# Kernel tuning notes

Measured on AMD Instinct MI355X. Metric: run time of the kernel, lower is better.

The kernel has to match this reference:

```python
import jax, jax.numpy as jnp
import numpy as np

B, P, E, D, A, M, V, T = 64, 196, 2048, 512, 512, 512, 10000, 31


def setup_inputs() -> dict:
    key = jax.random.key(0)
    ks = jax.random.split(key, 20)
    s = 0.02
    inp = {
        "encoder_out": jax.random.normal(ks[0], (B, P, E), jnp.float32),
        "captions": jax.random.randint(ks[1], (B, T), 0, V),
        "caption_lengths": jax.random.randint(ks[2], (B,), 2, T + 1).at[0].set(T),
        # parameters
        "W_emb": jax.random.normal(ks[3], (V, M), jnp.float32) * s,
        "We": jax.random.normal(ks[4], (A, E), jnp.float32) * s,
        "be": jnp.zeros((A,), jnp.float32),
        "Wd": jax.random.normal(ks[5], (A, D), jnp.float32) * s,
        "bd": jnp.zeros((A,), jnp.float32),
        "wf": jax.random.normal(ks[6], (1, A), jnp.float32) * s,
        "bf": jnp.zeros((1,), jnp.float32),
        "Wih": jax.random.normal(ks[7], (4 * D, M + E), jnp.float32) * s,
        "bih": jnp.zeros((4 * D,), jnp.float32),
        "Whh": jax.random.normal(ks[8], (4 * D, D), jnp.float32) * s,
        "bhh": jnp.zeros((4 * D,), jnp.float32),
        "Wfc": jax.random.normal(ks[9], (V, D), jnp.float32) * s,
        "bfc": jnp.zeros((V,), jnp.float32),
        "Wh0": jax.random.normal(ks[10], (D, E), jnp.float32) * s,
        "bh0": jnp.zeros((D,), jnp.float32),
        "Wc0": jax.random.normal(ks[11], (D, E), jnp.float32) * s,
        "bc0": jnp.zeros((D,), jnp.float32),
    }
    return inp


def _decode(encoder_out, W_emb, We, be, Wd, bd, wf, bf, Wih, bih, Whh, bhh,
            Wfc, bfc, Wh0, bh0, Wc0, bc0, captions, caption_lengths):
    # sort by length descending (matches torch .sort(descending=True))
    idx = jnp.argsort(-caption_lengths)
    lens = caption_lengths[idx]
    enc = encoder_out[idx]              # [B,P,E]
    caps = captions[idx]                # [B,T]
    emb = W_emb[caps]                   # [B,T,M]
    mean_enc = enc.mean(axis=1)         # [B,E]
    h0 = mean_enc @ Wh0.T + bh0         # [B,D]
    c0 = mean_enc @ Wc0.T + bc0
    dec_len = lens - 1                  # [B]
    att1 = enc @ We.T + be              # [B,P,A] precomputed encoder projection
    Tmax = caps.shape[1] - 1

    def step(carry, xs):
        h, c = carry
        e_t, t = xs                     # e_t: [B,M]
        active = (t < dec_len)          # [B]
        att2 = h @ Wd.T + bd            # [B,A]
        scores = jnp.tanh(att1 + att2[:, None, :]) @ wf[0] + bf[0]  # [B,P]
        alpha = jax.nn.softmax(scores, axis=-1)                      # [B,P]
        ctx = jnp.einsum('bp,bpe->be', alpha, enc)                   # [B,E]
        x = jnp.concatenate([e_t, ctx], axis=-1)                     # [B,M+E]
        gates = x @ Wih.T + bih + h @ Whh.T + bhh                    # [B,4D]
        i_g, f_g, g_g, o_g = jnp.split(gates, 4, axis=-1)
        c_t = jax.nn.sigmoid(f_g) * c + jax.nn.sigmoid(i_g) * jnp.tanh(g_g)
        h_t = jax.nn.sigmoid(o_g) * jnp.tanh(c_t)
        pred = h_t @ Wfc.T + bfc        # dropout in eval mode = identity
        m = active[:, None]
        h_new = jnp.where(m, h_t, h)
        c_new = jnp.where(m, c_t, c)
        pred = jnp.where(m, pred, 0.0)
        alpha = jnp.where(m, alpha, 0.0)
        return (h_new, c_new), (pred, alpha)

    emb_ts = jnp.swapaxes(emb[:, :Tmax, :], 0, 1)  # [Tmax,B,M]
    ts = jnp.arange(Tmax)
    _, (preds, alphas) = jax.lax.scan(step, (h0, c0), (emb_ts, ts))
    predictions = jnp.swapaxes(preds, 0, 1)   # [B,Tmax,V]
    alphas = jnp.swapaxes(alphas, 0, 1)       # [B,Tmax,P]
    return predictions, alphas


def reference(encoder_out, captions, caption_lengths, W_emb, We, be, Wd, bd,
              wf, bf, Wih, bih, Whh, bhh, Wfc, bfc, Wh0, bh0, Wc0, bc0):
    return _decode(encoder_out, W_emb, We, be, Wd, bd, wf, bf, Wih, bih,
                   Whh, bhh, Wfc, bfc, Wh0, bh0, Wc0, bc0,
                   captions, caption_lengths)
```

## Files before the change

kernel.cpp:

```cpp
#include <hip/hip_runtime.h>
#include <cstdint>
#include <cstddef>

typedef __attribute__((ext_vector_type(8))) short short8;
typedef __attribute__((ext_vector_type(4))) float f32x4;

#define DEV static __device__ __forceinline__

#define PRED_ELEMS 19200000ULL

#define OFF_ENC   0ULL
#define OFF_ATT1  51380224ULL
#define OFF_B1    64225280ULL
#define OFF_WFC   69468160ULL
#define OFF_WEB   79724544ULL
#define OFF_B0    81821696ULL
#define OFF_HH    81821696ULL
#define OFF_PA2   83787776ULL
#define OFF_B2    86016000ULL
#define OFF_HX    94404608ULL
#define OFF_C     94535680ULL
#define OFF_GEH   94797824ULL
#define OFF_SC    95322112ULL
#define OFF_CTX   95372288ULL
#define OFF_META  95634432ULL
#define OFF_ENCW  96000000ULL

DEV float b2f(unsigned short u){ unsigned v = ((unsigned)u) << 16; float f; __builtin_memcpy(&f, &v, 4); return f; }
DEV unsigned short f2b(float x){ unsigned v; __builtin_memcpy(&v, &x, 4); unsigned r = v + 0x7fffu + ((v >> 16) & 1u); return (unsigned short)(r >> 16); }
DEV float sigm(float x){ return 1.0f / (1.0f + __expf(-x)); }
DEV float tanhf_fast(float x){ float e = __expf(2.0f * x); return 1.0f - 2.0f / (e + 1.0f); }

DEV void gload16(const void* g, void* l){
  __builtin_amdgcn_global_load_lds((const __attribute__((address_space(1))) unsigned int*)g,
                                   (__attribute__((address_space(3))) unsigned int*)l, 16, 0, 0);
}

DEV void mm_core(const unsigned short* A, int ldA, int m0,
                 const unsigned short* Bm, int ldB, int n0,
                 int kIters, unsigned short* As, unsigned short* Bs, f32x4 acc[4])
{
  const int tid = threadIdx.x;
  const int lane = tid & 63, w = tid >> 6;
  const unsigned short* ga = A + (size_t)(m0 + lane) * ldA + w * 8;
  const unsigned short* gb = Bm + (size_t)(n0 + lane) * ldB + w * 8;
  unsigned short* la = As + w * 512;
  unsigned short* lb = Bs + w * 512;
  const int kb = lane >> 4, rr = lane & 15;
  for (int kk = 0; kk < kIters; ++kk) {
    gload16(ga, la); gload16(gb, lb);
    ga += 32; gb += 32;
    asm volatile("s_waitcnt vmcnt(0)" ::: "memory");
    __syncthreads();
    short8 bfr = *(const short8*)(Bs + (size_t)(kb * 64 + w * 16 + rr) * 8);
#pragma unroll
    for (int f = 0; f < 4; ++f) {
      short8 afr = *(const short8*)(As + (size_t)(kb * 64 + f * 16 + rr) * 8);
      acc[f] = __builtin_amdgcn_mfma_f32_16x16x32_bf16(afr, bfr, acc[f], 0, 0, 0);
    }
    __syncthreads();
  }
}

__global__ void k_meta(const int* __restrict__ caps, const int* __restrict__ lens, int* __restrict__ meta){
  int j = threadIdx.x;
  int lj = lens[j];
  int rank = 0;
  for (int k = 0; k < 64; ++k) { int lk = lens[k]; rank += (lk > lj) || (lk == lj && k < j); }
  meta[rank] = j; meta[64 + rank] = lj - 1;
  for (int t = 0; t < 31; ++t) meta[160 + rank * 31 + t] = caps[j * 31 + t];
  __syncthreads();
  if (j < 30) { int c = 0; for (int b = 0; b < 64; ++b) c += (meta[64 + b] > j); meta[128 + j] = c; }
}

__global__ __launch_bounds__(256) void k_encg(const float* __restrict__ enc, const int* __restrict__ meta, unsigned short* __restrict__ encb){
  int row = blockIdx.x; int b = row / 196, p = row % 196;
  const float* src = enc + ((size_t)meta[b] * 196 + p) * 2048;
  unsigned short* dst = encb + (size_t)row * 2048;
  int e0 = threadIdx.x * 8;
  short8 o;
#pragma unroll
  for (int j = 0; j < 8; ++j) o[j] = (short)f2b(src[e0 + j]);
  *(short8*)(dst + e0) = o;
}

__global__ __launch_bounds__(256) void k_wconv(const float* We, const float* Wh0, const float* Wc0,
                        const float* Wd, const float* Whh, const float* Wih, const float* Wfc,
                        unsigned short* Web, unsigned short* B0, unsigned short* B1,
                        unsigned short* Wfcb, unsigned short* B2){
  int bid = blockIdx.x, tid = threadIdx.x;
  if (bid < 512) {
    const float* s = We + (size_t)bid * 2048; unsigned short* d = Web + (size_t)bid * 2048;
    int e0 = tid * 8; short8 o;
#pragma unroll
    for (int j = 0; j < 8; ++j) o[j] = (short)f2b(s[e0 + j]);
    *(short8*)(d + e0) = o;
  } else if (bid < 1536) {
    int r = bid - 512;
    const float* s = (r < 512) ? (Wh0 + (size_t)r * 2048) : (Wc0 + (size_t)(r - 512) * 2048);
    unsigned short* d = B0 + (size_t)r * 2048;
    int e0 = tid * 8; short8 o;
#pragma unroll
    for (int j = 0; j < 8; ++j) o[j] = (short)f2b(s[e0 + j]);
    *(short8*)(d + e0) = o;
  } else if (bid < 3584) {
    int jr = bid - 1536; int g = (jr & 3) * 512 + (jr >> 2);
    const float* s = Wih + (size_t)g * 2560 + 512;
    unsigned short* d = B2 + (size_t)jr * 2048;
    int e0 = tid * 8; short8 o;
#pragma unroll
    for (int j = 0; j < 8; ++j) o[j] = (short)f2b(s[e0 + j]);
    *(short8*)(d + e0) = o;
  } else if (bid < 6144) {
    int n = bid - 3584; unsigned short* d = B1 + (size_t)n * 1024;
    int k0 = tid * 4;
    if (n < 512) {
#pragma unroll
      for (int j = 0; j < 4; ++j) { int k = k0 + j; d[k] = (k < 512) ? f2b(Wd[(size_t)n * 512 + k]) : (unsigned short)0; }
    } else {
      int j2 = n - 512; int g = (j2 & 3) * 512 + (j2 >> 2);
#pragma unroll
      for (int j = 0; j < 4; ++j) { int k = k0 + j;
        d[k] = (k < 512) ? f2b(Whh[(size_t)g * 512 + k]) : f2b(Wih[(size_t)g * 2560 + (k - 512)]); }
    }
  } else {
    int v = bid - 6144; unsigned short* d = Wfcb + (size_t)v * 512;
    int k0 = tid * 2;
#pragma unroll
    for (int j = 0; j < 2; ++j) d[k0 + j] = (v < 10000) ? f2b(Wfc[(size_t)v * 512 + k0 + j]) : (unsigned short)0;
  }
}

__global__ __launch_bounds__(256) void k_mean(const unsigned short* __restrict__ encb, unsigned short* __restrict__ meanb){
  int b = blockIdx.y, ch = blockIdx.x;
  int e = ch * 512 + threadIdx.x * 2;
  const unsigned short* ep = encb + (size_t)b * 196 * 2048 + e;
  float s0 = 0.f, s1 = 0.f;
  for (int p = 0; p < 196; ++p) {
    unsigned u = *(const unsigned*)(ep + (size_t)p * 2048);
    s0 += b2f((unsigned short)(u & 0xffff));
    s1 += b2f((unsigned short)(u >> 16));
  }
  const float inv = 1.0f / 196.0f;
  unsigned o = ((unsigned)f2b(s1 * inv) << 16) | f2b(s0 * inv);
  *(unsigned*)(meanb + (size_t)b * 2048 + e) = o;
}

__global__ __launch_bounds__(256) void k_h0c0(const unsigned short* meanb, const unsigned short* B0,
                      const float* bh0, const float* bc0, unsigned short* hx, float* cbuf){
  __shared__ __align__(16) unsigned short As[2048], Bs[2048];
  f32x4 acc[4];
#pragma unroll
  for (int f = 0; f < 4; ++f) acc[f] = (f32x4){0.f,0.f,0.f,0.f};
  int nt = blockIdx.x;
  mm_core(meanb, 2048, 0, B0, 2048, nt * 64, 64, As, Bs, acc);
  int lane = threadIdx.x & 63, w = threadIdx.x >> 6;
  int col = lane & 15, rhi = lane >> 4;
  int n = nt * 64 + w * 16 + col;
#pragma unroll
  for (int f = 0; f < 4; ++f)
#pragma unroll
    for (int r = 0; r < 4; ++r) {
      int b = f * 16 + rhi * 4 + r; float v = acc[f][r];
      if (n < 512) hx[(size_t)b * 1024 + n] = f2b(v + bh0[n]);
      else cbuf[(size_t)b * 512 + (n - 512)] = v + bc0[n - 512];
    }
}

__global__ void k_emb0(const float* __restrict__ Wemb, const int* __restrict__ meta, unsigned short* __restrict__ hx){
  int b = blockIdx.x;
  int cap = meta[160 + b * 31];
  for (int j = threadIdx.x; j < 512; j += 256)
    hx[(size_t)b * 1024 + 512 + j] = f2b(Wemb[(size_t)cap * 512 + j]);
}

__global__ __launch_bounds__(256) void k_att1(const unsigned short* __restrict__ encb,
                      const unsigned short* __restrict__ Web,
                      const float* __restrict__ be, unsigned short* __restrict__ att1b){
  __shared__ __align__(16) unsigned short As[2][4096], Bs[2][4096];
  int tid = threadIdx.x, lane = tid & 63, w = tid >> 6;
  int bid = blockIdx.x, mt, nt;
  if (bid < 384) { mt = (bid >> 5) * 8 + (bid & 7); nt = (bid >> 3) & 3; }
  else           { mt = 96 + ((bid - 384) >> 2);    nt = (bid - 384) & 3; }
  int wr = (w >> 1) * 64, wc = (w & 1) * 64;
  int rr = lane & 15, kb = lane >> 4;
  f32x4 acc[4][4];
#pragma unroll
  for (int f = 0; f < 4; ++f)
#pragma unroll
    for (int q = 0; q < 4; ++q) acc[f][q] = (f32x4){0.f,0.f,0.f,0.f};

  const unsigned short* gA = encb + (size_t)mt * 128 * 2048;
  const unsigned short* gB = Web + (size_t)nt * 128 * 2048;
  int L0 = tid, L1 = tid + 256;
  size_t s0 = (size_t)(L0 & 127) * 2048 + ((L0 >> 7) << 3);
  size_t s1 = (size_t)(L1 & 127) * 2048 + ((L1 >> 7) << 3);
  int d0 = (w * 64) * 8, d1 = (w * 64 + 256) * 8;

#define STAGE_A1(kk, bf) do { \
    gload16(gA + s0 + (size_t)(kk) * 32, &As[bf][d0]); \
    gload16(gB + s0 + (size_t)(kk) * 32, &Bs[bf][d0]); \
    gload16(gA + s1 + (size_t)(kk) * 32, &As[bf][d1]); \
    gload16(gB + s1 + (size_t)(kk) * 32, &Bs[bf][d1]); \
  } while (0)

  STAGE_A1(0, 0);
  __syncthreads();
  for (int kk = 0; kk < 64; ++kk) {
    int cur = kk & 1;
    if (kk < 63) STAGE_A1(kk + 1, cur ^ 1);
    short8 af[4], bq[4];
#pragma unroll
    for (int f = 0; f < 4; ++f)
      af[f] = *(const short8*)&As[cur][((kb << 7) + wr + f * 16 + rr) * 8];
#pragma unroll
    for (int q = 0; q < 4; ++q)
      bq[q] = *(const short8*)&Bs[cur][((kb << 7) + wc + q * 16 + rr) * 8];
#pragma unroll
    for (int f = 0; f < 4; ++f)
#pragma unroll
      for (int q = 0; q < 4; ++q)
        acc[f][q] = __builtin_amdgcn_mfma_f32_16x16x32_bf16(af[f], bq[q], acc[f][q], 0, 0, 0);
    __syncthreads();
  }
#undef STAGE_A1
  int col = lane & 15, rhi = lane >> 4;
#pragma unroll
  for (int q = 0; q < 4; ++q) {
    int n = nt * 128 + wc + q * 16 + col;
    float bev = be[n];
#pragma unroll
    for (int f = 0; f < 4; ++f)
#pragma unroll
      for (int r = 0; r < 4; ++r) {
        int m = mt * 128 + wr + f * 16 + rhi * 4 + r;
        att1b[(size_t)m * 512 + n] = f2b(acc[f][q][r] + bev);
      }
  }
}

__global__ __launch_bounds__(256) void k_encw(const unsigned short* __restrict__ encb,
                      const unsigned short* __restrict__ B2, unsigned short* __restrict__ encW){
  __shared__ __align__(16) unsigned short As[2][4096], Bs[2][4096];
  int tid = threadIdx.x, lane = tid & 63, w = tid >> 6;
  int xcd = blockIdx.x & 7, slot = blockIdx.x >> 3;
  int mtl = slot >> 4, nt = slot & 15;
  int mt = mtl * 8 + xcd;
  if (mt >= 98) return;
  int wr = (w >> 1) * 64, wc = (w & 1) * 64;
  int rr = lane & 15, kb = lane >> 4;
  f32x4 acc[4][4];
#pragma unroll
  for (int f = 0; f < 4; ++f)
#pragma unroll
    for (int q = 0; q < 4; ++q) acc[f][q] = (f32x4){0.f,0.f,0.f,0.f};

  const unsigned short* gA = encb + (size_t)mt * 128 * 2048;
  const unsigned short* gB = B2 + (size_t)nt * 128 * 2048;
  int L0 = tid, L1 = tid + 256;
  size_t s0 = (size_t)(L0 & 127) * 2048 + ((L0 >> 7) << 3);
  size_t s1 = (size_t)(L1 & 127) * 2048 + ((L1 >> 7) << 3);
  int d0 = (w * 64) * 8, d1 = (w * 64 + 256) * 8;

#define STAGE_W(kk, bf) do { \
    gload16(gA + s0 + (size_t)(kk) * 32, &As[bf][d0]); \
    gload16(gB + s0 + (size_t)(kk) * 32, &Bs[bf][d0]); \
    gload16(gA + s1 + (size_t)(kk) * 32, &As[bf][d1]); \
    gload16(gB + s1 + (size_t)(kk) * 32, &Bs[bf][d1]); \
  } while (0)

  STAGE_W(0, 0);
  __syncthreads();
  for (int kk = 0; kk < 64; ++kk) {
    int cur = kk & 1;
    if (kk < 63) STAGE_W(kk + 1, cur ^ 1);
    short8 af[4], bq[4];
#pragma unroll
    for (int f = 0; f < 4; ++f)
      af[f] = *(const short8*)&As[cur][((kb << 7) + wr + f * 16 + rr) * 8];
#pragma unroll
    for (int q = 0; q < 4; ++q)
      bq[q] = *(const short8*)&Bs[cur][((kb << 7) + wc + q * 16 + rr) * 8];
#pragma unroll
    for (int f = 0; f < 4; ++f)
#pragma unroll
      for (int q = 0; q < 4; ++q)
        acc[f][q] = __builtin_amdgcn_mfma_f32_16x16x32_bf16(af[f], bq[q], acc[f][q], 0, 0, 0);
    __syncthreads();
  }
#undef STAGE_W
  int col = lane & 15, rhi = lane >> 4;
#pragma unroll
  for (int q = 0; q < 4; ++q) {
    int n = nt * 128 + wc + q * 16 + col;
#pragma unroll
    for (int f = 0; f < 4; ++f)
#pragma unroll
      for (int r = 0; r < 4; ++r) {
        int m = mt * 128 + wr + f * 16 + rhi * 4 + r;
        encW[(size_t)m * 2048 + n] = f2b(acc[f][q][r]);
      }
  }
}

__global__ __launch_bounds__(256) void k_att2i(const unsigned short* __restrict__ hx,
                      const unsigned short* __restrict__ B1, float* __restrict__ pa2){
  int w = threadIdx.x >> 6, lane = threadIdx.x & 63;
  int omega = blockIdx.x * 4 + w;
  int rr = lane & 15, kb8 = (lane >> 4) * 8;
  const unsigned short* pb = B1 + (size_t)(omega * 16 + rr) * 1024 + kb8;
  const unsigned short* pa0 = hx + (size_t)rr * 1024 + kb8;
  f32x4 acc[4];
#pragma unroll
  for (int f = 0; f < 4; ++f) acc[f] = (f32x4){0.f,0.f,0.f,0.f};
#pragma unroll 4
  for (int kk = 0; kk < 16; ++kk) {
    short8 bfr = *(const short8*)(pb + kk * 32);
#pragma unroll
    for (int f = 0; f < 4; ++f) {
      short8 afr = *(const short8*)(pa0 + (size_t)f * 16384 + kk * 32);
      acc[f] = __builtin_amdgcn_mfma_f32_16x16x32_bf16(afr, bfr, acc[f], 0, 0, 0);
    }
  }
  int col = lane & 15, rhi = lane >> 4;
  int n = omega * 16 + col;
#pragma unroll
  for (int f = 0; f < 4; ++f)
#pragma unroll
    for (int r = 0; r < 4; ++r) { int b = f * 16 + rhi * 4 + r; pa2[(size_t)b * 512 + n] = acc[f][r]; }
}

__global__ __launch_bounds__(256) void k_scg(int t, const unsigned short* __restrict__ hx,
                      const unsigned short* __restrict__ B1, const unsigned short* __restrict__ att1b,
                      const float* __restrict__ pa2,
                      const float* __restrict__ bd, const float* __restrict__ bih, const float* __restrict__ bhh,
                      const float* __restrict__ wf, const float* __restrict__ bfp,
                      const int* __restrict__ meta,
                      float* __restrict__ geh, float* __restrict__ out, float* __restrict__ alp){
  int bid = blockIdx.x;
  int tid = threadIdx.x, lane = tid & 63, w = tid >> 6;
  int rr = lane & 15, kb8 = (lane >> 4) * 8;
  if (bid >= 64) {
    int jblk = bid - 64;
    const unsigned short* pb = B1 + (size_t)(512 + jblk * 16 + rr) * 1024 + kb8;
    const unsigned short* pa0 = hx + (size_t)rr * 1024 + kb8;
    f32x4 acc[4];
#pragma unroll
    for (int f = 0; f < 4; ++f) acc[f] = (f32x4){0.f,0.f,0.f,0.f};
#pragma unroll 4
    for (int kk = 0; kk < 32; ++kk) {
      short8 bfr = *(const short8*)(pb + kk * 32);
#pragma unroll
      for (int f = 0; f < 4; ++f) {
        short8 afr = *(const short8*)(pa0 + (size_t)f * 16384 + kk * 32);
        acc[f] = __builtin_amdgcn_mfma_f32_16x16x32_bf16(afr, bfr, acc[f], 0, 0, 0);
      }
    }
    int col = lane & 15, rhi = lane >> 4;
    int j = jblk * 16 + col; int g = (j & 3) * 512 + (j >> 2);
    float bv = bih[g] + bhh[g];
#pragma unroll
    for (int f = 0; f < 4; ++f)
#pragma unroll
      for (int r = 0; r < 4; ++r) { int b = f * 16 + rhi * 4 + r; geh[(size_t)b * 2048 + j] = acc[f][r] + bv; }
    return;
  }
  int b = bid;
  if (b >= meta[128 + t]) return;
  __shared__ float a2s[512];
  __shared__ float sal[200];
  __shared__ float red[256];
#pragma unroll
  for (int r = 0; r < 2; ++r) {
    int n = tid + r * 256;
    a2s[n] = pa2[(size_t)b * 512 + n] + pa2[(size_t)(64 + b) * 512 + n]
           + pa2[(size_t)(128 + b) * 512 + n] + pa2[(size_t)(192 + b) * 512 + n] + bd[n];
  }
  __syncthreads();
  {
    float wfr[8], a2[8];
#pragma unroll
    for (int j = 0; j < 8; ++j) { wfr[j] = wf[lane * 8 + j]; a2[j] = a2s[lane * 8 + j]; }
    float bf0 = bfp[0];
    for (int i = 0; i < 49; ++i) {
      int p = i * 4 + w;
      short8 av = *(const short8*)(att1b + ((size_t)(b * 196 + p)) * 512 + lane * 8);
      float s = 0.f;
#pragma unroll
      for (int j = 0; j < 8; ++j) s += tanhf_fast(b2f((unsigned short)av[j]) + a2[j]) * wfr[j];
#pragma unroll
      for (int off = 32; off; off >>= 1) s += __shfl_xor(s, off);
      if (lane == 0) sal[p] = s + bf0;
    }
  }
  __syncthreads();
  {
    float v = (tid < 196) ? sal[tid] : -3.0e38f;
    red[tid] = v; __syncthreads();
    for (int s = 128; s; s >>= 1) { if (tid < s) red[tid] = fmaxf(red[tid], red[tid + s]); __syncthreads(); }
    float mx = red[0]; __syncthreads();
    float ex = (tid < 196) ? __expf(v - mx) : 0.f;
    red[tid] = ex; __syncthreads();
    for (int s = 128; s; s >>= 1) { if (tid < s) red[tid] += red[tid + s]; __syncthreads(); }
    float inv = 1.0f / red[0];
    if (tid < 196) {
      float al = ex * inv;
      alp[(size_t)b * 196 + tid] = al;
      out[PRED_ELEMS + ((size_t)b * 30 + t) * 196 + tid] = al;
    }
  }
}

__global__ __launch_bounds__(256) void k_gc(int t, const float* __restrict__ alp,
                      const unsigned short* __restrict__ encW, const float* __restrict__ geh,
                      const unsigned short* __restrict__ B1,
                      const float* __restrict__ Wemb, const int* __restrict__ meta,
                      float* __restrict__ cbuf, unsigned short* __restrict__ hx,
                      unsigned short* __restrict__ hh, float* __restrict__ pa2){
  int b = blockIdx.y, ch = blockIdx.x;
  int tid = threadIdx.x, lane = tid & 63, w = tid >> 6;
  int na = meta[128 + t];
  __shared__ float sal[200];
  __shared__ float part[4][512];
  __shared__ float gt[512];
  __shared__ float hs[128];

  if (b < na) {
    if (tid < 196) sal[tid] = alp[(size_t)b * 196 + tid];
    __syncthreads();
    const unsigned short* ep = encW + ((size_t)b * 196) * 2048 + ch * 512 + lane * 8;
    float s8[8];
#pragma unroll
    for (int j = 0; j < 8; ++j) s8[j] = 0.f;
#pragma unroll 7
    for (int i = 0; i < 49; ++i) {
      int p = w + i * 4;
      short8 vv = *(const short8*)(ep + (size_t)p * 2048);
      float a = sal[p];
#pragma unroll
      for (int j = 0; j < 8; ++j) s8[j] += a * b2f((unsigned short)vv[j]);
    }
#pragma unroll
    for (int j = 0; j < 8; ++j) part[w][lane * 8 + j] = s8[j];
    __syncthreads();
    int j0 = tid * 2;
    gt[j0]     = part[0][j0] + part[1][j0] + part[2][j0] + part[3][j0]
               + geh[(size_t)b * 2048 + ch * 512 + j0];
    gt[j0 + 1] = part[0][j0 + 1] + part[1][j0 + 1] + part[2][j0 + 1] + part[3][j0 + 1]
               + geh[(size_t)b * 2048 + ch * 512 + j0 + 1];
    __syncthreads();

    if (tid < 128) {
      int d = ch * 128 + tid;
      float ig = gt[tid * 4 + 0];
      float fg = gt[tid * 4 + 1];
      float gg = gt[tid * 4 + 2];
      float og = gt[tid * 4 + 3];
      float c0 = cbuf[(size_t)b * 512 + d];
      float ct = sigm(fg) * c0 + sigm(ig) * tanhf_fast(gg);
      float ht = sigm(og) * tanhf_fast(ct);
      cbuf[(size_t)b * 512 + d] = ct;
      unsigned short hb = f2b(ht);
      hs[tid] = b2f(hb);
      hx[(size_t)b * 1024 + d] = hb;
      hh[((size_t)t * 64 + b) * 512 + d] = hb;
      int cap = meta[160 + b * 31 + t + 1];
      hx[(size_t)b * 1024 + 512 + d] = f2b(Wemb[(size_t)cap * 512 + d]);
    }
  } else {
    if (tid < 128) {
      int d = ch * 128 + tid;
      unsigned short hold = hx[(size_t)b * 1024 + d];
      hs[tid] = b2f(hold);
      hh[((size_t)t * 64 + b) * 512 + d] = hold;
      int cap = meta[160 + b * 31 + t + 1];
      hx[(size_t)b * 1024 + 512 + d] = f2b(Wemb[(size_t)cap * 512 + d]);
    }
  }
  __syncthreads();
#pragma unroll
  for (int r = 0; r < 2; ++r) {
    int n = tid + r * 256;
    const unsigned short* wp = B1 + (size_t)n * 1024 + ch * 128;
    float s = 0.f;
#pragma unroll
    for (int kk = 0; kk < 16; ++kk) {
      short8 wv = *(const short8*)(wp + kk * 8);
#pragma unroll
      for (int j = 0; j < 8; ++j) s += hs[kk * 8 + j] * b2f((unsigned short)wv[j]);
    }
    pa2[((size_t)ch * 64 + b) * 512 + n] = s;
  }
}

__global__ __launch_bounds__(256) void k_pred(const unsigned short* __restrict__ hh,
                      const unsigned short* __restrict__ Wfcb, const float* __restrict__ bfc,
                      const int* __restrict__ meta, float* __restrict__ out){
  __shared__ __align__(16) unsigned short As[2][4096], Bs[2][4096];
  int tid = threadIdx.x, lane = tid & 63, w = tid >> 6;
  int mt = blockIdx.x % 15, nt = blockIdx.x / 15;
  int wr = (w >> 1) * 64, wc = (w & 1) * 64;
  int rr = lane & 15, kb = lane >> 4;
  f32x4 acc[4][4];
#pragma unroll
  for (int f = 0; f < 4; ++f)
#pragma unroll
    for (int q = 0; q < 4; ++q) acc[f][q] = (f32x4){0.f,0.f,0.f,0.f};

  const unsigned short* gA = hh + (size_t)mt * 128 * 512;
  int L0 = tid, L1 = tid + 256;
  size_t sa0 = (size_t)(L0 & 127) * 512 + ((L0 >> 7) << 3);
  size_t sa1 = (size_t)(L1 & 127) * 512 + ((L1 >> 7) << 3);
  int br0 = nt * 128 + (L0 & 127); if (br0 > 10015) br0 = 10015;
  int br1 = nt * 128 + (L1 & 127); if (br1 > 10015) br1 = 10015;
  size_t sb0 = (size_t)br0 * 512 + ((L0 >> 7) << 3);
  size_t sb1 = (size_t)br1 * 512 + ((L1 >> 7) << 3);
  int d0 = (w * 64) * 8, d1 = (w * 64 + 256) * 8;

#define STAGE_P(kk, bf) do { \
    gload16(gA + sa0 + (size_t)(kk) * 32, &As[bf][d0]); \
    gload16(Wfcb + sb0 + (size_t)(kk) * 32, &Bs[bf][d0]); \
    gload16(gA + sa1 + (size_t)(kk) * 32, &As[bf][d1]); \
    gload16(Wfcb + sb1 + (size_t)(kk) * 32, &Bs[bf][d1]); \
  } while (0)

  STAGE_P(0, 0);
  __syncthreads();
  for (int kk = 0; kk < 16; ++kk) {
    int cur = kk & 1;
    if (kk < 15) STAGE_P(kk + 1, cur ^ 1);
    short8 af[4], bq[4];
#pragma unroll
    for (int f = 0; f < 4; ++f)
      af[f] = *(const short8*)&As[cur][((kb << 7) + wr + f * 16 + rr) * 8];
#pragma unroll
    for (int q = 0; q < 4; ++q)
      bq[q] = *(const short8*)&Bs[cur][((kb << 7) + wc + q * 16 + rr) * 8];
#pragma unroll
    for (int f = 0; f < 4; ++f)
#pragma unroll
      for (int q = 0; q < 4; ++q)
        acc[f][q] = __builtin_amdgcn_mfma_f32_16x16x32_bf16(af[f], bq[q], acc[f][q], 0, 0, 0);
    __syncthreads();
  }
#undef STAGE_P
  int col = lane & 15, rhi = lane >> 4;
  int tt = mt * 2 + (wr >> 6);
  int na = meta[128 + tt];
#pragma unroll
  for (int q = 0; q < 4; ++q) {
    int n = nt * 128 + wc + q * 16 + col;
    if (n >= 10000) continue;
    float bv = bfc[n];
#pragma unroll
    for (int f = 0; f < 4; ++f)
#pragma unroll
      for (int r = 0; r < 4; ++r) {
        int b = f * 16 + rhi * 4 + r;
        if (b < na) out[(size_t)b * 300000 + (size_t)tt * 10000 + n] = acc[f][q][r] + bv;
      }
  }
}

extern "C" void kernel_launch(void* const* d_in, const int* in_sizes, int n_in,
                              void* d_out, int out_size, void* d_ws, size_t ws_size,
                              hipStream_t stream) {
  (void)in_sizes; (void)n_in; (void)ws_size;
  const float* enc  = (const float*)d_in[0];
  const int*   caps = (const int*)d_in[1];
  const int*   lens = (const int*)d_in[2];
  const float* Wemb = (const float*)d_in[3];
  const float* We   = (const float*)d_in[4];
  const float* be   = (const float*)d_in[5];
  const float* Wd   = (const float*)d_in[6];
  const float* bd   = (const float*)d_in[7];
  const float* wf   = (const float*)d_in[8];
  const float* bf   = (const float*)d_in[9];
  const float* Wih  = (const float*)d_in[10];
  const float* bih  = (const float*)d_in[11];
  const float* Whh  = (const float*)d_in[12];
  const float* bhh  = (const float*)d_in[13];
  const float* Wfc  = (const float*)d_in[14];
  const float* bfc  = (const float*)d_in[15];
  const float* Wh0  = (const float*)d_in[16];
  const float* bh0  = (const float*)d_in[17];
  const float* Wc0  = (const float*)d_in[18];
  const float* bc0  = (const float*)d_in[19];

  char* ws = (char*)d_ws;
  unsigned short* encb  = (unsigned short*)(ws + OFF_ENC);
  unsigned short* att1b = (unsigned short*)(ws + OFF_ATT1);
  unsigned short* B1    = (unsigned short*)(ws + OFF_B1);
  unsigned short* Wfcb  = (unsigned short*)(ws + OFF_WFC);
  unsigned short* Web   = (unsigned short*)(ws + OFF_WEB);
  unsigned short* B0    = (unsigned short*)(ws + OFF_B0);
  unsigned short* hh    = (unsigned short*)(ws + OFF_HH);
  float*          pa2   = (float*)(ws + OFF_PA2);
  unsigned short* B2    = (unsigned short*)(ws + OFF_B2);
  unsigned short* hx    = (unsigned short*)(ws + OFF_HX);
  float*          cbuf  = (float*)(ws + OFF_C);
  float*          geh   = (float*)(ws + OFF_GEH);
  float*          sc    = (float*)(ws + OFF_SC);
  unsigned short* ctxb  = (unsigned short*)(ws + OFF_CTX);
  int*            meta  = (int*)(ws + OFF_META);
  unsigned short* encWb = (unsigned short*)(ws + OFF_ENCW);
  unsigned short* meanb = ctxb;
  float* out = (float*)d_out;

  hipMemsetAsync(d_out, 0, (size_t)out_size * sizeof(float), stream);
  k_meta<<<1, 64, 0, stream>>>(caps, lens, meta);
  k_encg<<<12544, 256, 0, stream>>>(enc, meta, encb);
  k_wconv<<<16160, 256, 0, stream>>>(We, Wh0, Wc0, Wd, Whh, Wih, Wfc, Web, B0, B1, Wfcb, B2);
  k_mean<<<dim3(4, 64), 256, 0, stream>>>(encb, meanb);
  k_h0c0<<<16, 256, 0, stream>>>(meanb, B0, bh0, bc0, hx, cbuf);
  k_emb0<<<64, 256, 0, stream>>>(Wemb, meta, hx);
  hipMemsetAsync(pa2 + 64 * 512, 0, 3 * 64 * 512 * sizeof(float), stream);
  k_att2i<<<8, 256, 0, stream>>>(hx, B1, pa2);
  k_att1<<<392, 256, 0, stream>>>(encb, Web, be, att1b);
  k_encw<<<1664, 256, 0, stream>>>(encb, B2, encWb);

  for (int t = 0; t < 30; ++t) {
    k_scg<<<192, 256, 0, stream>>>(t, hx, B1, att1b, pa2, bd, bih, bhh, wf, bf, meta, geh, out, sc);
    k_gc<<<dim3(4, 64), 256, 0, stream>>>(t, sc, encWb, geh, B1, Wemb, meta, cbuf, hx, hh, pa2);
  }
  k_pred<<<1185, 256, 0, stream>>>(hh, Wfcb, bfc, meta, out);
}
```

Measured before the change: 2.117 ms.

## Fuse att1 and encW GEMMs into one launch; use MFMA for per-step pa2 projection

Merges the encoder attention projection GEMM and the encoder-weight GEMM into a single kernel that shares the encoder A tile and picks its B matrix and epilogue by N-tile index, with XCD-aware tile mapping. This saves one launch and improves load balance and L2 reuse of the encoder rows. In the per-step gate kernel, the scalar dot-product loop for the pa2 partial projection is replaced by bf16 MFMA using a broadcast h vector. Only column 0 of each MFMA output is kept, so the matrix units do some wasted work, but this replaces a long serial FMA chain.

```diff
diff --git a/kernel.cpp b/kernel.cpp
--- a/kernel.cpp
+++ b/kernel.cpp
@@ -174,14 +174,16 @@
     hx[(size_t)b * 1024 + 512 + j] = f2b(Wemb[(size_t)cap * 512 + j]);
 }
 
-__global__ __launch_bounds__(256) void k_att1(const unsigned short* __restrict__ encb,
-                      const unsigned short* __restrict__ Web,
-                      const float* __restrict__ be, unsigned short* __restrict__ att1b){
+__global__ __launch_bounds__(256) void k_big(const unsigned short* __restrict__ encb,
+                      const unsigned short* __restrict__ Web, const unsigned short* __restrict__ B2,
+                      const float* __restrict__ be,
+                      unsigned short* __restrict__ att1b, unsigned short* __restrict__ encW){
   __shared__ __align__(16) unsigned short As[2][4096], Bs[2][4096];
   int tid = threadIdx.x, lane = tid & 63, w = tid >> 6;
-  int bid = blockIdx.x, mt, nt;
-  if (bid < 384) { mt = (bid >> 5) * 8 + (bid & 7); nt = (bid >> 3) & 3; }
-  else           { mt = 96 + ((bid - 384) >> 2);    nt = (bid - 384) & 3; }
+  int xcd = blockIdx.x & 7, slot = blockIdx.x >> 3;
+  int mtl = slot / 20, nt = slot % 20;
+  int mt = mtl * 8 + xcd;
+  if (mt >= 98) return;
   int wr = (w >> 1) * 64, wc = (w & 1) * 64;
   int rr = lane & 15, kb = lane >> 4;
   f32x4 acc[4][4];
@@ -191,24 +193,25 @@
     for (int q = 0; q < 4; ++q) acc[f][q] = (f32x4){0.f,0.f,0.f,0.f};
 
   const unsigned short* gA = encb + (size_t)mt * 128 * 2048;
-  const unsigned short* gB = Web + (size_t)nt * 128 * 2048;
+  const unsigned short* gB = (nt < 4) ? (Web + (size_t)nt * 128 * 2048)
+                                      : (B2 + (size_t)(nt - 4) * 128 * 2048);
   int L0 = tid, L1 = tid + 256;
   size_t s0 = (size_t)(L0 & 127) * 2048 + ((L0 >> 7) << 3);
   size_t s1 = (size_t)(L1 & 127) * 2048 + ((L1 >> 7) << 3);
   int d0 = (w * 64) * 8, d1 = (w * 64 + 256) * 8;
 
-#define STAGE_A1(kk, bf) do { \
+#define STAGE_B(kk, bf) do { \
     gload16(gA + s0 + (size_t)(kk) * 32, &As[bf][d0]); \
     gload16(gB + s0 + (size_t)(kk) * 32, &Bs[bf][d0]); \
     gload16(gA + s1 + (size_t)(kk) * 32, &As[bf][d1]); \
     gload16(gB + s1 + (size_t)(kk) * 32, &Bs[bf][d1]); \
   } while (0)
 
-  STAGE_A1(0, 0);
+  STAGE_B(0, 0);
   __syncthreads();
   for (int kk = 0; kk < 64; ++kk) {
     int cur = kk & 1;
-    if (kk < 63) STAGE_A1(kk + 1, cur ^ 1);
+    if (kk < 63) STAGE_B(kk + 1, cur ^ 1);
     short8 af[4], bq[4];
 #pragma unroll
     for (int f = 0; f < 4; ++f)
@@ -223,83 +226,33 @@
         acc[f][q] = __builtin_amdgcn_mfma_f32_16x16x32_bf16(af[f], bq[q], acc[f][q], 0, 0, 0);
     __syncthreads();
   }
-#undef STAGE_A1
+#undef STAGE_B
   int col = lane & 15, rhi = lane >> 4;
-#pragma unroll
-  for (int q = 0; q < 4; ++q) {
-    int n = nt * 128 + wc + q * 16 + col;
-    float bev = be[n];
-#pragma unroll
-    for (int f = 0; f < 4; ++f)
-#pragma unroll
-      for (int r = 0; r < 4; ++r) {
-        int m = mt * 128 + wr + f * 16 + rhi * 4 + r;
-        att1b[(size_t)m * 512 + n] = f2b(acc[f][q][r] + bev);
-      }
-  }
-}
-
-__global__ __launch_bounds__(256) void k_encw(const unsigned short* __restrict__ encb,
-                      const unsigned short* __restrict__ B2, unsigned short* __restrict__ encW){
-  __shared__ __align__(16) unsigned short As[2][4096], Bs[2][4096];
-  int tid = threadIdx.x, lane = tid & 63, w = tid >> 6;
-  int xcd = blockIdx.x & 7, slot = blockIdx.x >> 3;
-  int mtl = slot >> 4, nt = slot & 15;
-  int mt = mtl * 8 + xcd;
-  if (mt >= 98) return;
-  int wr = (w >> 1) * 64, wc = (w & 1) * 64;
-  int rr = lane & 15, kb = lane >> 4;
-  f32x4 acc[4][4];
-#pragma unroll
-  for (int f = 0; f < 4; ++f)
-#pragma unroll
-    for (int q = 0; q < 4; ++q) acc[f][q] = (f32x4){0.f,0.f,0.f,0.f};
-
-  const unsigned short* gA = encb + (size_t)mt * 128 * 2048;
-  const unsigned short* gB = B2 + (size_t)nt * 128 * 2048;
-  int L0 = tid, L1 = tid + 256;
-  size_t s0 = (size_t)(L0 & 127) * 2048 + ((L0 >> 7) << 3);
-  size_t s1 = (size_t)(L1 & 127) * 2048 + ((L1 >> 7) << 3);
-  int d0 = (w * 64) * 8, d1 = (w * 64 + 256) * 8;
-
-#define STAGE_W(kk, bf) do { \
-    gload16(gA + s0 + (size_t)(kk) * 32, &As[bf][d0]); \
-    gload16(gB + s0 + (size_t)(kk) * 32, &Bs[bf][d0]); \
-    gload16(gA + s1 + (size_t)(kk) * 32, &As[bf][d1]); \
-    gload16(gB + s1 + (size_t)(kk) * 32, &Bs[bf][d1]); \
-  } while (0)
-
-  STAGE_W(0, 0);
-  __syncthreads();
-  for (int kk = 0; kk < 64; ++kk) {
-    int cur = kk & 1;
-    if (kk < 63) STAGE_W(kk + 1, cur ^ 1);
-    short8 af[4], bq[4];
-#pragma unroll
-    for (int f = 0; f < 4; ++f)
-      af[f] = *(const short8*)&As[cur][((kb << 7) + wr + f * 16 + rr) * 8];
-#pragma unroll
-    for (int q = 0; q < 4; ++q)
-      bq[q] = *(const short8*)&Bs[cur][((kb << 7) + wc + q * 16 + rr) * 8];
-#pragma unroll
-    for (int f = 0; f < 4; ++f)
-#pragma unroll
-      for (int q = 0; q < 4; ++q)
-        acc[f][q] = __builtin_amdgcn_mfma_f32_16x16x32_bf16(af[f], bq[q], acc[f][q], 0, 0, 0);
-    __syncthreads();
-  }
-#undef STAGE_W
-  int col = lane & 15, rhi = lane >> 4;
-#pragma unroll
-  for (int q = 0; q < 4; ++q) {
-    int n = nt * 128 + wc + q * 16 + col;
-#pragma unroll
-    for (int f = 0; f < 4; ++f)
-#pragma unroll
-      for (int r = 0; r < 4; ++r) {
-        int m = mt * 128 + wr + f * 16 + rhi * 4 + r;
-        encW[(size_t)m * 2048 + n] = f2b(acc[f][q][r]);
-      }
+  if (nt < 4) {
+#pragma unroll
+    for (int q = 0; q < 4; ++q) {
+      int n = nt * 128 + wc + q * 16 + col;
+      float bev = be[n];
+#pragma unroll
+      for (int f = 0; f < 4; ++f)
+#pragma unroll
+        for (int r = 0; r < 4; ++r) {
+          int m = mt * 128 + wr + f * 16 + rhi * 4 + r;
+          att1b[(size_t)m * 512 + n] = f2b(acc[f][q][r] + bev);
+        }
+    }
+  } else {
+#pragma unroll
+    for (int q = 0; q < 4; ++q) {
+      int n = (nt - 4) * 128 + wc + q * 16 + col;
+#pragma unroll
+      for (int f = 0; f < 4; ++f)
+#pragma unroll
+        for (int r = 0; r < 4; ++r) {
+          int m = mt * 128 + wr + f * 16 + rhi * 4 + r;
+          encW[(size_t)m * 2048 + n] = f2b(acc[f][q][r]);
+        }
+    }
   }
 }
 
@@ -423,7 +376,7 @@
   __shared__ float sal[200];
   __shared__ float part[4][512];
   __shared__ float gt[512];
-  __shared__ float hs[128];
+  __shared__ __align__(16) unsigned short hsb[128];
 
   if (b < na) {
     if (tid < 196) sal[tid] = alp[(size_t)b * 196 + tid];
@@ -461,7 +414,7 @@
       float ht = sigm(og) * tanhf_fast(ct);
       cbuf[(size_t)b * 512 + d] = ct;
       unsigned short hb = f2b(ht);
-      hs[tid] = b2f(hb);
+      hsb[tid] = hb;
       hx[(size_t)b * 1024 + d] = hb;
       hh[((size_t)t * 64 + b) * 512 + d] = hb;
       int cap = meta[160 + b * 31 + t + 1];
@@ -471,25 +424,33 @@
     if (tid < 128) {
       int d = ch * 128 + tid;
       unsigned short hold = hx[(size_t)b * 1024 + d];
-      hs[tid] = b2f(hold);
+      hsb[tid] = hold;
       hh[((size_t)t * 64 + b) * 512 + d] = hold;
       int cap = meta[160 + b * 31 + t + 1];
       hx[(size_t)b * 1024 + 512 + d] = f2b(Wemb[(size_t)cap * 512 + d]);
     }
   }
   __syncthreads();
-#pragma unroll
-  for (int r = 0; r < 2; ++r) {
-    int n = tid + r * 256;
-    const unsigned short* wp = B1 + (size_t)n * 1024 + ch * 128;
-    float s = 0.f;
-#pragma unroll
-    for (int kk = 0; kk < 16; ++kk) {
-      short8 wv = *(const short8*)(wp + kk * 8);
-#pragma unroll
-      for (int j = 0; j < 8; ++j) s += hs[kk * 8 + j] * b2f((unsigned short)wv[j]);
-    }
-    pa2[((size_t)ch * 64 + b) * 512 + n] = s;
+  {
+    int rr = lane & 15, kb8 = (lane >> 4) * 8;
+    f32x4 pacc[8];
+#pragma unroll
+    for (int q = 0; q < 8; ++q) pacc[q] = (f32x4){0.f,0.f,0.f,0.f};
+#pragma unroll
+    for (int kk = 0; kk < 4; ++kk) {
+      short8 afr = *(const short8*)(hsb + kk * 32 + kb8);
+#pragma unroll
+      for (int q = 0; q < 8; ++q) {
+        const unsigned short* bp = B1 + (size_t)(w * 128 + q * 16 + rr) * 1024 + ch * 128 + kk * 32 + kb8;
+        short8 bfr = *(const short8*)bp;
+        pacc[q] = __builtin_amdgcn_mfma_f32_16x16x32_bf16(afr, bfr, pacc[q], 0, 0, 0);
+      }
+    }
+    if (lane < 16) {
+      float* pd = pa2 + ((size_t)ch * 64 + b) * 512 + w * 128 + lane;
+#pragma unroll
+      for (int q = 0; q < 8; ++q) pd[q * 16] = pacc[q][0];
+    }
   }
 }
 
@@ -616,8 +577,7 @@
   k_emb0<<<64, 256, 0, stream>>>(Wemb, meta, hx);
   hipMemsetAsync(pa2 + 64 * 512, 0, 3 * 64 * 512 * sizeof(float), stream);
   k_att2i<<<8, 256, 0, stream>>>(hx, B1, pa2);
-  k_att1<<<392, 256, 0, stream>>>(encb, Web, be, att1b);
-  k_encw<<<1664, 256, 0, stream>>>(encb, B2, encWb);
+  k_big<<<2080, 256, 0, stream>>>(encb, Web, B2, be, att1b, encWb);
 
   for (int t = 0; t < 30; ++t) {
     k_scg<<<192, 256, 0, stream>>>(t, hx, B1, att1b, pa2, bd, bih, bhh, wf, bf, meta, geh, out, sc);
```

After: 2.071 ms. 2.1% less time.
